# Kernel optimization log

Measured on AMD Instinct MI355X. Metric: run time of the kernel, lower is better.

The kernel has to match this reference:

```python
import jax, jax.numpy as jnp
import numpy as np
from jax import lax

N_CLUSTERS = 512
B = 128


def _extract_windows(sym, k, s):
    # sym: (B, H, W, C) int symbols -> (B, oh, ow, k*k*C); window layout (ki, kj, c)
    Bb, H, W, C = sym.shape
    oh = (H - k) // s + 1
    ow = (W - k) // s + 1
    parts = [sym[:, i:i + s * oh:s, j:j + s * ow:s, :] for i in range(k) for j in range(k)]
    w = jnp.stack(parts, axis=3)  # (B, oh, ow, k*k, C)
    return w.reshape(Bb, oh, ow, k * k * C)


def _conv_reduce(arr, add_lut):
    # Faithful SymConv2D inner reduction: sort window symbols, then sequentially
    # fold through add_lut with the conditional swap-and-resort of the original.
    n = arr.shape[1]
    arr = jnp.sort(arr, axis=1)
    tmp = arr[:, 0]

    def step(carry, j):
        a, t = carry
        t2 = add_lut[a[:, j], t]
        jc = jnp.minimum(j + 1, n - 1)
        nxt = a[:, jc]
        cond = (j < n - 2) & (t2 > nxt)
        a_sw = a.at[:, jc].set(jnp.where(cond, t2, nxt))
        a_new = jnp.where(cond[:, None], jnp.sort(a_sw, axis=1), a)
        t_new = jnp.where(cond, nxt, t2)
        return (a_new, t_new), None

    (_, tmp), _ = lax.scan(step, (arr, tmp), jnp.arange(1, n))
    return tmp


def _fc_reduce(arr, add_lut):
    # SymFC inner reduction: sort once, then plain sequential add_lut fold.
    arr = jnp.sort(arr, axis=1)
    cols = jnp.moveaxis(arr[:, 1:], 1, 0)  # (n-1, R)

    def step(t, col):
        return add_lut[col, t], None

    tmp, _ = lax.scan(step, arr[:, 0], cols)
    return tmp


def _sym_conv(sym, w_sym, conv_lut, add_lut, bias_lut, k=5, s=2):
    # sym: (B, H, W, C) int symbols; w_sym: (k*k*C, Co) kernel symbols
    win = _extract_windows(sym, k, s)  # (B, oh, ow, n)
    Bb, oh, ow, n = win.shape
    Co = w_sym.shape[1]
    # conv_lut gather: pair each window symbol with each output channel's kernel symbol
    g = conv_lut[win[:, :, :, None, :], w_sym.T[None, None, None, :, :]]  # (B, oh, ow, Co, n)
    syms = _conv_reduce(g.reshape(-1, n), add_lut).reshape(Bb, oh, ow, Co)
    return bias_lut[syms, jnp.arange(Co)]


def _sym_fc(x, w_sym, fc_lut, add_lut, bias_lut):
    # x: (B, n) symbols; w_sym: (m, n)
    g = fc_lut[x[:, None, :], w_sym[None, :, :]]  # (B, m, n)
    Bb, m, n = g.shape
    syms = _fc_reduce(g.reshape(-1, n), add_lut).reshape(Bb, m)
    return bias_lut[syms, jnp.arange(m)]


def _discretize(x, centroid_lut):
    # 1x1 patches: nearest-centroid quantization of each pixel
    px = x[:, 0]  # (B, 32, 32)
    d = jnp.abs(px[..., None] - centroid_lut[None, None, None, :, 0])
    return lax.stop_gradient(jnp.argmin(d, axis=-1).astype(jnp.int32))


def setup_inputs() -> dict:
    key = jax.random.key(0)
    ks = jax.random.split(key, 16)
    ri = lambda k, shape: jax.random.randint(k, shape, 0, N_CLUSTERS, dtype=jnp.int32)
    return {
        'x_bat': jax.random.normal(ks[0], (B, 1, 32, 32), jnp.float32),
        'centroid_lut': jax.random.normal(ks[1], (N_CLUSTERS, 1), jnp.float32),
        'conv_lut': ri(ks[2], (N_CLUSTERS, N_CLUSTERS)),
        'fc_lut': ri(ks[3], (N_CLUSTERS, N_CLUSTERS)),
        'add_lut': ri(ks[4], (N_CLUSTERS, N_CLUSTERS)),
        'relu_lut': ri(ks[5], (N_CLUSTERS,)),
        'c1_bias_lut': ri(ks[6], (N_CLUSTERS, 6)),
        'c2_bias_lut': ri(ks[7], (N_CLUSTERS, 16)),
        'f1_bias_lut': ri(ks[8], (N_CLUSTERS, 120)),
        'f2_bias_lut': ri(ks[9], (N_CLUSTERS, 84)),
        'c1f': ri(ks[10], (25, 6)),
        'c2f': ri(ks[11], (150, 16)),
        'f1f': ri(ks[12], (120, 400)),
        'f2f': ri(ks[13], (84, 120)),
        'fc3_w': jax.random.normal(ks[14], (10, 84), jnp.float32) * 0.1,
        'fc3_b': jax.random.normal(ks[15], (10,), jnp.float32) * 0.1,
    }


def reference(x_bat, centroid_lut, conv_lut, fc_lut, add_lut, relu_lut,
              c1_bias_lut, c2_bias_lut, f1_bias_lut, f2_bias_lut,
              c1f, c2f, f1f, f2f, fc3_w, fc3_b):
    x = _discretize(x_bat, centroid_lut)[..., None]              # (B, 32, 32, 1)
    x = _sym_conv(x, c1f, conv_lut, add_lut, c1_bias_lut)        # (B, 14, 14, 6)
    x = relu_lut[x]
    x = _sym_conv(x, c2f, conv_lut, add_lut, c2_bias_lut)        # (B, 5, 5, 16)
    x = relu_lut[x]
    # symbolic_to_symbolic_win with 1x1 patches is identity; channels-first flatten (permute(2,0,1))
    x = jnp.transpose(x, (0, 3, 1, 2)).reshape(x.shape[0], 400)  # (B, 400)
    x = relu_lut[_sym_fc(x, f1f, fc_lut, add_lut, f1_bias_lut)]  # (B, 120)
    x = relu_lut[_sym_fc(x, f2f, fc_lut, add_lut, f2_bias_lut)]  # (B, 84)
    feats = centroid_lut[x, 0]                                   # symbols -> floats, (B, 84)
    logits = feats @ fc3_w.T + fc3_b
    return jax.nn.softmax(logits, axis=1)


if __name__ == '__main__':
    out = reference(**setup_inputs())
    print(out.shape, out.dtype)
```

## Files before the change

### kernel.cpp

```cpp
#include <hip/hip_runtime.h>

#define NC 512

__global__ __launch_bounds__(256) void k_transpose_pack2(
    const int* __restrict__ srcA, unsigned short* __restrict__ dstA,
    const int* __restrict__ srcB, unsigned short* __restrict__ dstB)
{
    __shared__ unsigned short tile[64][65];
    int bid = blockIdx.x & 63;
    const int* src = (blockIdx.x < 64) ? srcA : srcB;
    unsigned short* dst = (blockIdx.x < 64) ? dstA : dstB;
    int tx = bid % 8, ty = bid / 8;
    int lane = threadIdx.x & 63, grp = threadIdx.x >> 6;
    for (int r = grp * 16; r < grp * 16 + 16; ++r)
        tile[r][lane] = (unsigned short)src[(ty * 64 + r) * NC + tx * 64 + lane];
    __syncthreads();
    for (int r = grp * 16; r < grp * 16 + 16; ++r)
        dst[(tx * 64 + r) * NC + ty * 64 + lane] = tile[lane][r];
}

__global__ __launch_bounds__(256) void k_discretize(
    const float* __restrict__ x, const float* __restrict__ cent,
    unsigned short* __restrict__ out)
{
    __shared__ float c[NC];
    int tid = threadIdx.x;
    for (int i = tid; i < NC; i += 256) c[i] = cent[i];
    __syncthreads();
    int id = blockIdx.x * 256 + tid;
    float px = x[id];
    float best = fabsf(px - c[0]);
    int bi = 0;
    for (int k = 1; k < NC; ++k) {
        float d = fabsf(px - c[k]);
        if (d < best) { best = d; bi = k; }
    }
    out[id] = (unsigned short)bi;
}

template<int INST>
struct ScanL {
    uint32_t* col;
    uint64_t w0, w1;
    uint32_t mask;
    int chunk;

    __device__ inline void init(uint32_t* c) { col = c; mask = 0; chunk = -1; }
    __device__ inline void load() {
        uint32_t a0 = col[(chunk * 4 + 0) * INST];
        uint32_t a1 = col[(chunk * 4 + 1) * INST];
        uint32_t a2 = col[(chunk * 4 + 2) * INST];
        uint32_t a3 = col[(chunk * 4 + 3) * INST];
        mask = col[(64 + chunk) * INST];
        w0 = ((uint64_t)a1 << 32) | a0;
        w1 = ((uint64_t)a3 << 32) | a2;
    }
    __device__ inline void ensure() { while (mask == 0) { ++chunk; load(); } }
    __device__ inline int  peek()   { ensure(); return chunk * 32 + (int)__builtin_ctz(mask); }
    __device__ inline void consume_min() {
        int k = (int)__builtin_ctz(mask);
        int sh = (k & 15) << 2;
        bool hi = k >= 16;
        uint64_t cw = hi ? w1 : w0;
        uint32_t cnt = (uint32_t)(cw >> sh) & 0xFu;
        cw -= (1ull << sh);
        if (hi) w1 = cw; else w0 = cw;
        if (cnt == 1) mask &= ~(1u << k);
    }
    __device__ inline int pop() { int v = peek(); consume_min(); return v; }
    __device__ inline void insert(int v) {
        int rel = v - chunk * 32;
        if (rel < 32) {
            int sh = (rel & 15) << 2;
            bool hi = rel >= 16;
            uint64_t cw = hi ? w1 : w0;
            cw += (1ull << sh);
            if (hi) w1 = cw; else w0 = cw;
            mask |= (1u << rel);
        } else {
            col[(v >> 3) * INST] += (1u << ((v & 7) << 2));
            col[(64 + (v >> 5)) * INST] |= (1u << (v & 31));
        }
    }
};

template<typename IT, typename OT, bool KMAJOR, int INST,
         int CIN, int CO, int IH, int IW, int OH, int OW>
__device__ __forceinline__ void conv_body(
    const IT* __restrict__ in_sym,
    const int* __restrict__ wsym,
    const unsigned short* __restrict__ convT,
    const int* __restrict__ add_lut,
    const int* __restrict__ bias_lut,
    const int* __restrict__ relu_lut,
    OT* __restrict__ out)
{
    constexpr int N    = 25 * CIN;
    constexpr int SUB  = 64 / INST;
    constexpr int PPI  = OH * OW;
    constexpr int BPC  = (128 * PPI) / INST;
    __shared__ uint32_t bins[80 * INST];
    int tid = threadIdx.x;
    int il  = tid % INST;
    int sub = tid / INST;

    for (int i = tid; i < 80 * INST; i += 64) bins[i] = 0u;

    int posg = blockIdx.x % BPC;
    int co   = blockIdx.x / BPC;
    int pos  = posg * INST + il;
    int b  = pos / PPI;
    int yx = pos % PPI;
    int oy = yx / OW, ox = yx % OW;
    __syncthreads();

#pragma unroll 4
    for (int n = sub; n < N; n += SUB) {
        int i   = n / (5 * CIN);
        int rem = n % (5 * CIN);
        int j   = rem / CIN;
        int c   = rem % CIN;
        int s = (int)in_sym[((b * IH + (oy * 2 + i)) * IW + (ox * 2 + j)) * CIN + c];
        int w = wsym[n * CO + co];
        int g = convT[w * NC + s];
        atomicAdd(&bins[(g >> 3) * INST + il], 1u << ((g & 7) << 2));
        atomicOr (&bins[(64 + (g >> 5)) * INST + il], 1u << (g & 31));
    }
    __syncthreads();

    ScanL<INST> sc; sc.init(bins + il);
    int t = sc.pop();
    int u = sc.pop();
    int v = sc.pop();
    int t2 = add_lut[u * NC + t];
#pragma unroll 1
    for (int j = 1; j <= N - 3; ++j) {
        int bb = sc.pop();
        bool cA = (t2 <= v);
        bool cC = (t2 > bb);
        t = cA ? t2 : v;
        u = cA ? v : (cC ? bb : t2);
        int t2n = add_lut[u * NC + t];
        __builtin_amdgcn_sched_barrier(0);
        if (cC) { sc.insert(t2); v = sc.pop(); }
        else    v = bb;
        t2 = t2n;
    }
    t = t2;
    t = add_lut[v * NC + t];
    if (sub == 0) {
        int r = relu_lut[bias_lut[t * CO + co]];
        if (KMAJOR) out[(co * PPI + yx) * 128 + b] = (OT)r;
        else        out[pos * CO + co] = (OT)r;
    }
}

__global__ __launch_bounds__(64) void k_conv1(
    const unsigned short* in, const int* wsym, const unsigned short* convT,
    const int* add_lut, const int* bias, const int* relu, unsigned short* out)
{
    conv_body<unsigned short, unsigned short, false, 64, 1, 6, 32, 32, 14, 14>(
        in, wsym, convT, add_lut, bias, relu, out);
}

__global__ __launch_bounds__(64) void k_conv2(
    const unsigned short* in, const int* wsym, const unsigned short* convT,
    const int* add_lut, const int* bias, const int* relu, int* out)
{
    conv_body<unsigned short, int, true, 16, 6, 16, 14, 14, 5, 5>(
        in, wsym, convT, add_lut, bias, relu, out);
}

template<int M, int K>
__device__ __forceinline__ void fc_body(
    const int* __restrict__ in_sym,
    const int* __restrict__ wsym,
    const unsigned short* __restrict__ fcT,
    const int* __restrict__ add_lut,
    const int* __restrict__ bias_lut,
    const int* __restrict__ relu_lut,
    int* __restrict__ out)
{
    constexpr int INST = 8;
    constexpr int SUB  = 8;
    __shared__ uint32_t bins[80 * INST];
    int tid = threadIdx.x;
    int il  = tid % INST;
    int sub = tid / INST;

    for (int i = tid; i < 80 * INST; i += 64) bins[i] = 0u;

    int m  = blockIdx.x / 16;
    int bg = blockIdx.x % 16;
    int b  = bg * INST + il;
    __syncthreads();

#pragma unroll 4
    for (int k = sub; k < K; k += SUB) {
        int x = in_sym[k * 128 + b];
        int w = wsym[m * K + k];
        int g = fcT[w * NC + x];
        atomicAdd(&bins[(g >> 3) * INST + il], 1u << ((g & 7) << 2));
        atomicOr (&bins[(64 + (g >> 5)) * INST + il], 1u << (g & 31));
    }
    __syncthreads();

    ScanL<INST> sc; sc.init(bins + il);
    int t = sc.pop();
    int x = sc.pop();
    int t2 = add_lut[x * NC + t];
#pragma unroll 1
    for (int s = 1; s < K - 1; ++s) {
        int xn = sc.pop();
        t = t2;
        t2 = add_lut[xn * NC + t];
        __builtin_amdgcn_sched_barrier(0);
    }
    t = t2;
    if (sub == 0)
        out[m * 128 + b] = relu_lut[bias_lut[t * M + m]];
}

__global__ __launch_bounds__(64) void k_fc1(
    const int* in, const int* wsym, const unsigned short* fcT,
    const int* add_lut, const int* bias, const int* relu, int* out)
{
    fc_body<120, 400>(in, wsym, fcT, add_lut, bias, relu, out);
}

__global__ __launch_bounds__(64) void k_fc2(
    const int* in, const int* wsym, const unsigned short* fcT,
    const int* add_lut, const int* bias, const int* relu, int* out)
{
    fc_body<84, 120>(in, wsym, fcT, add_lut, bias, relu, out);
}

__global__ __launch_bounds__(64) void k_head(
    const int* __restrict__ f2m,
    const float* __restrict__ cent,
    const float* __restrict__ w,
    const float* __restrict__ bias,
    float* __restrict__ out)
{
    int b = blockIdx.x * 64 + threadIdx.x;
    float acc[10];
#pragma unroll
    for (int o = 0; o < 10; ++o) acc[o] = bias[o];
    for (int k = 0; k < 84; ++k) {
        float f = cent[f2m[k * 128 + b]];
#pragma unroll
        for (int o = 0; o < 10; ++o) acc[o] += f * w[o * 84 + k];
    }
    float mx = acc[0];
#pragma unroll
    for (int o = 1; o < 10; ++o) mx = fmaxf(mx, acc[o]);
    float s = 0.f;
#pragma unroll
    for (int o = 0; o < 10; ++o) { acc[o] = expf(acc[o] - mx); s += acc[o]; }
    float inv = 1.f / s;
#pragma unroll
    for (int o = 0; o < 10; ++o) out[b * 10 + o] = acc[o] * inv;
}

extern "C" void kernel_launch(void* const* d_in, const int* in_sizes, int n_in,
                              void* d_out, int out_size, void* d_ws, size_t ws_size,
                              hipStream_t stream)
{
    const float* x_bat  = (const float*)d_in[0];
    const float* cent   = (const float*)d_in[1];
    const int* conv_lut = (const int*)d_in[2];
    const int* fc_lut   = (const int*)d_in[3];
    const int* add_lut  = (const int*)d_in[4];
    const int* relu_lut = (const int*)d_in[5];
    const int* c1_bias  = (const int*)d_in[6];
    const int* c2_bias  = (const int*)d_in[7];
    const int* f1_bias  = (const int*)d_in[8];
    const int* f2_bias  = (const int*)d_in[9];
    const int* c1f      = (const int*)d_in[10];
    const int* c2f      = (const int*)d_in[11];
    const int* f1f      = (const int*)d_in[12];
    const int* f2f      = (const int*)d_in[13];
    const float* fc3_w  = (const float*)d_in[14];
    const float* fc3_b  = (const float*)d_in[15];
    float* out = (float*)d_out;

    char* ws = (char*)d_ws;
    unsigned short* convT = (unsigned short*)(ws);
    unsigned short* fcT   = (unsigned short*)(ws + 524288);
    unsigned short* sym0  = (unsigned short*)(ws + 1048576);
    unsigned short* c1o   = (unsigned short*)(ws + 1310720);
    int* c2o = (int*)(ws + 1611776);
    int* f1o = (int*)(ws + 1816576);
    int* f2o = (int*)(ws + 1878016);

    k_transpose_pack2<<<128, 256, 0, stream>>>(conv_lut, convT, fc_lut, fcT);
    k_discretize<<<512, 256, 0, stream>>>(x_bat, cent, sym0);
    k_conv1<<<2352, 64, 0, stream>>>(sym0, c1f, convT, add_lut, c1_bias, relu_lut, c1o);
    k_conv2<<<3200, 64, 0, stream>>>(c1o, c2f, convT, add_lut, c2_bias, relu_lut, c2o);
    k_fc1<<<1920, 64, 0, stream>>>(c2o, f1f, fcT, add_lut, f1_bias, relu_lut, f1o);
    k_fc2<<<1344, 64, 0, stream>>>(f1o, f2f, fcT, add_lut, f2_bias, relu_lut, f2o);
    k_head<<<2, 64, 0, stream>>>(f2o, cent, fc3_w, fc3_b, out);
}
```

Baseline: 381.0 us.

## Interleave two independent reduction chains per thread in conv2 and FC kernels

Each thread in conv2, fc1 and fc2 now handles two output instances (A and B) and interleaves their sequential add_lut fold chains. The aim is to hide the latency of the dependent global LUT loads by giving each wavefront two independent chains, while halving the grid sizes. In exchange, each block uses twice the shared memory, registers rise, and there are half as many blocks, which could lower occupancy or leave the GPU underfilled.

```diff
diff --git a/kernel.cpp b/kernel.cpp
--- a/kernel.cpp
+++ b/kernel.cpp
@@ -38,7 +38,7 @@
     out[id] = (unsigned short)bi;
 }
 
-template<int INST>
+template<int STRIDE>
 struct ScanL {
     uint32_t* col;
     uint64_t w0, w1;
@@ -47,11 +47,11 @@
 
     __device__ inline void init(uint32_t* c) { col = c; mask = 0; chunk = -1; }
     __device__ inline void load() {
-        uint32_t a0 = col[(chunk * 4 + 0) * INST];
-        uint32_t a1 = col[(chunk * 4 + 1) * INST];
-        uint32_t a2 = col[(chunk * 4 + 2) * INST];
-        uint32_t a3 = col[(chunk * 4 + 3) * INST];
-        mask = col[(64 + chunk) * INST];
+        uint32_t a0 = col[(chunk * 4 + 0) * STRIDE];
+        uint32_t a1 = col[(chunk * 4 + 1) * STRIDE];
+        uint32_t a2 = col[(chunk * 4 + 2) * STRIDE];
+        uint32_t a3 = col[(chunk * 4 + 3) * STRIDE];
+        mask = col[(64 + chunk) * STRIDE];
         w0 = ((uint64_t)a1 << 32) | a0;
         w1 = ((uint64_t)a3 << 32) | a2;
     }
@@ -78,21 +78,18 @@
             if (hi) w1 = cw; else w0 = cw;
             mask |= (1u << rel);
         } else {
-            col[(v >> 3) * INST] += (1u << ((v & 7) << 2));
-            col[(64 + (v >> 5)) * INST] |= (1u << (v & 31));
+            col[(v >> 3) * STRIDE] += (1u << ((v & 7) << 2));
+            col[(64 + (v >> 5)) * STRIDE] |= (1u << (v & 31));
         }
     }
 };
 
 template<typename IT, typename OT, bool KMAJOR, int INST,
          int CIN, int CO, int IH, int IW, int OH, int OW>
-__device__ __forceinline__ void conv_body(
-    const IT* __restrict__ in_sym,
-    const int* __restrict__ wsym,
-    const unsigned short* __restrict__ convT,
-    const int* __restrict__ add_lut,
-    const int* __restrict__ bias_lut,
-    const int* __restrict__ relu_lut,
+__device__ __forceinline__ void conv_body1(
+    const IT* __restrict__ in_sym, const int* __restrict__ wsym,
+    const unsigned short* __restrict__ convT, const int* __restrict__ add_lut,
+    const int* __restrict__ bias_lut, const int* __restrict__ relu_lut,
     OT* __restrict__ out)
 {
     constexpr int N    = 25 * CIN;
@@ -155,11 +152,99 @@
     }
 }
 
+template<typename IT, typename OT, bool KMAJOR, int INST,
+         int CIN, int CO, int IH, int IW, int OH, int OW>
+__device__ __forceinline__ void conv_body2(
+    const IT* __restrict__ in_sym, const int* __restrict__ wsym,
+    const unsigned short* __restrict__ convT, const int* __restrict__ add_lut,
+    const int* __restrict__ bias_lut, const int* __restrict__ relu_lut,
+    OT* __restrict__ out)
+{
+    constexpr int N    = 25 * CIN;
+    constexpr int SUB  = 64 / INST;
+    constexpr int PPI  = OH * OW;
+    constexpr int CH   = 2 * INST;
+    constexpr int BPC  = (128 * PPI) / CH;
+    __shared__ uint32_t bins[80 * CH];
+    int tid = threadIdx.x;
+    int il  = tid % INST;
+    int sub = tid / INST;
+
+    for (int i = tid; i < 80 * CH; i += 64) bins[i] = 0u;
+
+    int posg = blockIdx.x % BPC;
+    int co   = blockIdx.x / BPC;
+    int posA = posg * CH + il;
+    int posB = posg * CH + INST + il;
+    int bA = posA / PPI, yxA = posA % PPI, oyA = yxA / OW, oxA = yxA % OW;
+    int bB = posB / PPI, yxB = posB % PPI, oyB = yxB / OW, oxB = yxB % OW;
+    __syncthreads();
+
+#pragma unroll 2
+    for (int n = sub; n < N; n += SUB) {
+        int i   = n / (5 * CIN);
+        int rem = n % (5 * CIN);
+        int j   = rem / CIN;
+        int c   = rem % CIN;
+        int w = wsym[n * CO + co];
+        int sA = (int)in_sym[((bA * IH + (oyA * 2 + i)) * IW + (oxA * 2 + j)) * CIN + c];
+        int gA = convT[w * NC + sA];
+        atomicAdd(&bins[(gA >> 3) * CH + il], 1u << ((gA & 7) << 2));
+        atomicOr (&bins[(64 + (gA >> 5)) * CH + il], 1u << (gA & 31));
+        int sB = (int)in_sym[((bB * IH + (oyB * 2 + i)) * IW + (oxB * 2 + j)) * CIN + c];
+        int gB = convT[w * NC + sB];
+        atomicAdd(&bins[(gB >> 3) * CH + INST + il], 1u << ((gB & 7) << 2));
+        atomicOr (&bins[(64 + (gB >> 5)) * CH + INST + il], 1u << (gB & 31));
+    }
+    __syncthreads();
+
+    ScanL<CH> scA; scA.init(bins + il);
+    ScanL<CH> scB; scB.init(bins + INST + il);
+    int tA = scA.pop(), uA = scA.pop(), vA = scA.pop();
+    int t2A = add_lut[uA * NC + tA];
+    int tB = scB.pop(), uB = scB.pop(), vB = scB.pop();
+    int t2B = add_lut[uB * NC + tB];
+#pragma unroll 1
+    for (int j = 1; j <= N - 3; ++j) {
+        int bbA = scA.pop();
+        bool cAA = (t2A <= vA), cCA = (t2A > bbA);
+        tA = cAA ? t2A : vA;
+        uA = cAA ? vA : (cCA ? bbA : t2A);
+        int t2nA = add_lut[uA * NC + tA];
+        __builtin_amdgcn_sched_barrier(0);
+        if (cCA) { scA.insert(t2A); vA = scA.pop(); }
+        else     vA = bbA;
+        t2A = t2nA;
+        int bbB = scB.pop();
+        bool cAB = (t2B <= vB), cCB = (t2B > bbB);
+        tB = cAB ? t2B : vB;
+        uB = cAB ? vB : (cCB ? bbB : t2B);
+        int t2nB = add_lut[uB * NC + tB];
+        __builtin_amdgcn_sched_barrier(0);
+        if (cCB) { scB.insert(t2B); vB = scB.pop(); }
+        else     vB = bbB;
+        t2B = t2nB;
+    }
+    tA = t2A; tA = add_lut[vA * NC + tA];
+    tB = t2B; tB = add_lut[vB * NC + tB];
+    if (sub == 0) {
+        int rA = relu_lut[bias_lut[tA * CO + co]];
+        int rB = relu_lut[bias_lut[tB * CO + co]];
+        if (KMAJOR) {
+            out[(co * PPI + yxA) * 128 + bA] = (OT)rA;
+            out[(co * PPI + yxB) * 128 + bB] = (OT)rB;
+        } else {
+            out[posA * CO + co] = (OT)rA;
+            out[posB * CO + co] = (OT)rB;
+        }
+    }
+}
+
 __global__ __launch_bounds__(64) void k_conv1(
     const unsigned short* in, const int* wsym, const unsigned short* convT,
     const int* add_lut, const int* bias, const int* relu, unsigned short* out)
 {
-    conv_body<unsigned short, unsigned short, false, 64, 1, 6, 32, 32, 14, 14>(
+    conv_body1<unsigned short, unsigned short, false, 64, 1, 6, 32, 32, 14, 14>(
         in, wsym, convT, add_lut, bias, relu, out);
 }
 
@@ -167,7 +252,7 @@
     const unsigned short* in, const int* wsym, const unsigned short* convT,
     const int* add_lut, const int* bias, const int* relu, int* out)
 {
-    conv_body<unsigned short, int, true, 16, 6, 16, 14, 14, 5, 5>(
+    conv_body2<unsigned short, int, true, 16, 6, 16, 14, 14, 5, 5>(
         in, wsym, convT, add_lut, bias, relu, out);
 }
 
@@ -182,43 +267,59 @@
     int* __restrict__ out)
 {
     constexpr int INST = 8;
+    constexpr int CH   = 16;
     constexpr int SUB  = 8;
-    __shared__ uint32_t bins[80 * INST];
+    __shared__ uint32_t bins[80 * CH];
     int tid = threadIdx.x;
     int il  = tid % INST;
     int sub = tid / INST;
 
-    for (int i = tid; i < 80 * INST; i += 64) bins[i] = 0u;
-
-    int m  = blockIdx.x / 16;
-    int bg = blockIdx.x % 16;
-    int b  = bg * INST + il;
-    __syncthreads();
-
-#pragma unroll 4
+    for (int i = tid; i < 80 * CH; i += 64) bins[i] = 0u;
+
+    int m  = blockIdx.x / 8;
+    int bg = blockIdx.x % 8;
+    int bA = bg * CH + il;
+    int bB = bg * CH + INST + il;
+    __syncthreads();
+
+#pragma unroll 2
     for (int k = sub; k < K; k += SUB) {
-        int x = in_sym[k * 128 + b];
         int w = wsym[m * K + k];
-        int g = fcT[w * NC + x];
-        atomicAdd(&bins[(g >> 3) * INST + il], 1u << ((g & 7) << 2));
-        atomicOr (&bins[(64 + (g >> 5)) * INST + il], 1u << (g & 31));
-    }
-    __syncthreads();
-
-    ScanL<INST> sc; sc.init(bins + il);
-    int t = sc.pop();
-    int x = sc.pop();
-    int t2 = add_lut[x * NC + t];
+        int xA = in_sym[k * 128 + bA];
+        int gA = fcT[w * NC + xA];
+        atomicAdd(&bins[(gA >> 3) * CH + il], 1u << ((gA & 7) << 2));
+        atomicOr (&bins[(64 + (gA >> 5)) * CH + il], 1u << (gA & 31));
+        int xB = in_sym[k * 128 + bB];
+        int gB = fcT[w * NC + xB];
+        atomicAdd(&bins[(gB >> 3) * CH + INST + il], 1u << ((gB & 7) << 2));
+        atomicOr (&bins[(64 + (gB >> 5)) * CH + INST + il], 1u << (gB & 31));
+    }
+    __syncthreads();
+
+    ScanL<CH> scA; scA.init(bins + il);
+    ScanL<CH> scB; scB.init(bins + INST + il);
+    int tA = scA.pop();
+    int xA = scA.pop();
+    int t2A = add_lut[xA * NC + tA];
+    int tB = scB.pop();
+    int xB = scB.pop();
+    int t2B = add_lut[xB * NC + tB];
 #pragma unroll 1
     for (int s = 1; s < K - 1; ++s) {
-        int xn = sc.pop();
-        t = t2;
-        t2 = add_lut[xn * NC + t];
+        int xnA = scA.pop();
+        tA = t2A;
+        t2A = add_lut[xnA * NC + tA];
         __builtin_amdgcn_sched_barrier(0);
-    }
-    t = t2;
-    if (sub == 0)
-        out[m * 128 + b] = relu_lut[bias_lut[t * M + m]];
+        int xnB = scB.pop();
+        tB = t2B;
+        t2B = add_lut[xnB * NC + tB];
+        __builtin_amdgcn_sched_barrier(0);
+    }
+    tA = t2A; tB = t2B;
+    if (sub == 0) {
+        out[m * 128 + bA] = relu_lut[bias_lut[tA * M + m]];
+        out[m * 128 + bB] = relu_lut[bias_lut[tB * M + m]];
+    }
 }
 
 __global__ __launch_bounds__(64) void k_fc1(
@@ -296,8 +397,8 @@
     k_transpose_pack2<<<128, 256, 0, stream>>>(conv_lut, convT, fc_lut, fcT);
     k_discretize<<<512, 256, 0, stream>>>(x_bat, cent, sym0);
     k_conv1<<<2352, 64, 0, stream>>>(sym0, c1f, convT, add_lut, c1_bias, relu_lut, c1o);
-    k_conv2<<<3200, 64, 0, stream>>>(c1o, c2f, convT, add_lut, c2_bias, relu_lut, c2o);
-    k_fc1<<<1920, 64, 0, stream>>>(c2o, f1f, fcT, add_lut, f1_bias, relu_lut, f1o);
-    k_fc2<<<1344, 64, 0, stream>>>(f1o, f2f, fcT, add_lut, f2_bias, relu_lut, f2o);
+    k_conv2<<<1600, 64, 0, stream>>>(c1o, c2f, convT, add_lut, c2_bias, relu_lut, c2o);
+    k_fc1<<<960, 64, 0, stream>>>(c2o, f1f, fcT, add_lut, f1_bias, relu_lut, f1o);
+    k_fc2<<<672, 64, 0, stream>>>(f1o, f2f, fcT, add_lut, f2_bias, relu_lut, f2o);
     k_head<<<2, 64, 0, stream>>>(f2o, cent, fc3_w, fc3_b, out);
 }
```

Result: slower. 479.4 us (+25.8%).

## Merge preprocessing kernels and prefetch next histogram chunk in conv scan

Applied to the files above, without the earlier changes.

Fuses the LUT transpose and discretize kernels into one launch split by block index, saving one launch. In the conv reduction, a new scanner prefetches the next 32-symbol chunk of the LDS histogram into registers so the chunk advance does not wait on a fresh LDS read. Out-of-chunk inserts now go through atomics issued only by the leader lane, and the prefetch is refreshed when the insert lands in the next chunk. This adds register pressure and subtle correctness coupling between the lanes that share a histogram column.

```diff
diff --git a/kernel.cpp b/kernel.cpp
--- a/kernel.cpp
+++ b/kernel.cpp
@@ -2,44 +2,44 @@
 
 #define NC 512
 
-__global__ __launch_bounds__(256) void k_transpose_pack2(
+__global__ __launch_bounds__(256) void k_pre(
     const int* __restrict__ srcA, unsigned short* __restrict__ dstA,
-    const int* __restrict__ srcB, unsigned short* __restrict__ dstB)
-{
-    __shared__ unsigned short tile[64][65];
-    int bid = blockIdx.x & 63;
-    const int* src = (blockIdx.x < 64) ? srcA : srcB;
-    unsigned short* dst = (blockIdx.x < 64) ? dstA : dstB;
-    int tx = bid % 8, ty = bid / 8;
-    int lane = threadIdx.x & 63, grp = threadIdx.x >> 6;
-    for (int r = grp * 16; r < grp * 16 + 16; ++r)
-        tile[r][lane] = (unsigned short)src[(ty * 64 + r) * NC + tx * 64 + lane];
-    __syncthreads();
-    for (int r = grp * 16; r < grp * 16 + 16; ++r)
-        dst[(tx * 64 + r) * NC + ty * 64 + lane] = tile[lane][r];
-}
-
-__global__ __launch_bounds__(256) void k_discretize(
+    const int* __restrict__ srcB, unsigned short* __restrict__ dstB,
     const float* __restrict__ x, const float* __restrict__ cent,
-    unsigned short* __restrict__ out)
-{
-    __shared__ float c[NC];
+    unsigned short* __restrict__ outsym)
+{
+    __shared__ __align__(16) char smem[64 * 65 * 2];
     int tid = threadIdx.x;
-    for (int i = tid; i < NC; i += 256) c[i] = cent[i];
-    __syncthreads();
-    int id = blockIdx.x * 256 + tid;
-    float px = x[id];
-    float best = fabsf(px - c[0]);
-    int bi = 0;
-    for (int k = 1; k < NC; ++k) {
-        float d = fabsf(px - c[k]);
-        if (d < best) { best = d; bi = k; }
-    }
-    out[id] = (unsigned short)bi;
-}
-
-template<int INST>
-struct ScanL {
+    if (blockIdx.x < 128) {
+        unsigned short (*tile)[65] = (unsigned short(*)[65])smem;
+        int bid = blockIdx.x & 63;
+        const int* src = (blockIdx.x < 64) ? srcA : srcB;
+        unsigned short* dst = (blockIdx.x < 64) ? dstA : dstB;
+        int tx = bid % 8, ty = bid / 8;
+        int lane = tid & 63, grp = tid >> 6;
+        for (int r = grp * 16; r < grp * 16 + 16; ++r)
+            tile[r][lane] = (unsigned short)src[(ty * 64 + r) * NC + tx * 64 + lane];
+        __syncthreads();
+        for (int r = grp * 16; r < grp * 16 + 16; ++r)
+            dst[(tx * 64 + r) * NC + ty * 64 + lane] = tile[lane][r];
+    } else {
+        float* c = (float*)smem;
+        for (int i = tid; i < NC; i += 256) c[i] = cent[i];
+        __syncthreads();
+        int id = (blockIdx.x - 128) * 256 + tid;
+        float px = x[id];
+        float best = fabsf(px - c[0]);
+        int bi = 0;
+        for (int k = 1; k < NC; ++k) {
+            float d = fabsf(px - c[k]);
+            if (d < best) { best = d; bi = k; }
+        }
+        outsym[id] = (unsigned short)bi;
+    }
+}
+
+template<int STRIDE>
+struct ScanL32 {
     uint32_t* col;
     uint64_t w0, w1;
     uint32_t mask;
@@ -47,11 +47,11 @@
 
     __device__ inline void init(uint32_t* c) { col = c; mask = 0; chunk = -1; }
     __device__ inline void load() {
-        uint32_t a0 = col[(chunk * 4 + 0) * INST];
-        uint32_t a1 = col[(chunk * 4 + 1) * INST];
-        uint32_t a2 = col[(chunk * 4 + 2) * INST];
-        uint32_t a3 = col[(chunk * 4 + 3) * INST];
-        mask = col[(64 + chunk) * INST];
+        uint32_t a0 = col[(chunk * 4 + 0) * STRIDE];
+        uint32_t a1 = col[(chunk * 4 + 1) * STRIDE];
+        uint32_t a2 = col[(chunk * 4 + 2) * STRIDE];
+        uint32_t a3 = col[(chunk * 4 + 3) * STRIDE];
+        mask = col[(64 + chunk) * STRIDE];
         w0 = ((uint64_t)a1 << 32) | a0;
         w1 = ((uint64_t)a3 << 32) | a2;
     }
@@ -68,6 +68,49 @@
         if (cnt == 1) mask &= ~(1u << k);
     }
     __device__ inline int pop() { int v = peek(); consume_min(); return v; }
+};
+
+template<int STRIDE>
+struct ScanP {
+    uint32_t* col;
+    uint64_t w0, w1;
+    uint32_t mask;
+    uint32_t p0, p1, p2, p3, pm;
+    int chunk;
+    bool leader;
+
+    __device__ inline void pf(int nc) {
+        p0 = col[(nc * 4 + 0) * STRIDE];
+        p1 = col[(nc * 4 + 1) * STRIDE];
+        p2 = col[(nc * 4 + 2) * STRIDE];
+        p3 = col[(nc * 4 + 3) * STRIDE];
+        pm = col[(64 + nc) * STRIDE];
+    }
+    __device__ inline void init(uint32_t* c, bool lead) {
+        col = c; leader = lead; mask = 0; chunk = -1;
+        pf(0);
+    }
+    __device__ inline void advance() {
+        ++chunk;
+        w0 = ((uint64_t)p1 << 32) | p0;
+        w1 = ((uint64_t)p3 << 32) | p2;
+        mask = pm;
+        int nc = chunk + 1;
+        if (nc < 16) pf(nc);
+    }
+    __device__ inline void ensure() { while (mask == 0) advance(); }
+    __device__ inline int  peek()   { ensure(); return chunk * 32 + (int)__builtin_ctz(mask); }
+    __device__ inline void consume_min() {
+        int k = (int)__builtin_ctz(mask);
+        int sh = (k & 15) << 2;
+        bool hi = k >= 16;
+        uint64_t cw = hi ? w1 : w0;
+        uint32_t cnt = (uint32_t)(cw >> sh) & 0xFu;
+        cw -= (1ull << sh);
+        if (hi) w1 = cw; else w0 = cw;
+        if (cnt == 1) mask &= ~(1u << k);
+    }
+    __device__ inline int pop() { int v = peek(); consume_min(); return v; }
     __device__ inline void insert(int v) {
         int rel = v - chunk * 32;
         if (rel < 32) {
@@ -78,8 +121,11 @@
             if (hi) w1 = cw; else w0 = cw;
             mask |= (1u << rel);
         } else {
-            col[(v >> 3) * INST] += (1u << ((v & 7) << 2));
-            col[(64 + (v >> 5)) * INST] |= (1u << (v & 31));
+            if (leader) {
+                atomicAdd(&col[(v >> 3) * STRIDE], 1u << ((v & 7) << 2));
+                atomicOr (&col[(64 + (v >> 5)) * STRIDE], 1u << (v & 31));
+            }
+            if (rel < 64) pf(chunk + 1);
         }
     }
 };
@@ -128,7 +174,7 @@
     }
     __syncthreads();
 
-    ScanL<INST> sc; sc.init(bins + il);
+    ScanP<INST> sc; sc.init(bins + il, sub == 0);
     int t = sc.pop();
     int u = sc.pop();
     int v = sc.pop();
@@ -205,7 +251,7 @@
     }
     __syncthreads();
 
-    ScanL<INST> sc; sc.init(bins + il);
+    ScanL32<INST> sc; sc.init(bins + il);
     int t = sc.pop();
     int x = sc.pop();
     int t2 = add_lut[x * NC + t];
@@ -293,8 +339,7 @@
     int* f1o = (int*)(ws + 1816576);
     int* f2o = (int*)(ws + 1878016);
 
-    k_transpose_pack2<<<128, 256, 0, stream>>>(conv_lut, convT, fc_lut, fcT);
-    k_discretize<<<512, 256, 0, stream>>>(x_bat, cent, sym0);
+    k_pre<<<640, 256, 0, stream>>>(conv_lut, convT, fc_lut, fcT, x_bat, cent, sym0);
     k_conv1<<<2352, 64, 0, stream>>>(sym0, c1f, convT, add_lut, c1_bias, relu_lut, c1o);
     k_conv2<<<3200, 64, 0, stream>>>(c1o, c2f, convT, add_lut, c2_bias, relu_lut, c2o);
     k_fc1<<<1920, 64, 0, stream>>>(c2o, f1f, fcT, add_lut, f1_bias, relu_lut, f1o);
```

Measured after the change: 392.1 us. 1.03x slower.

## Merge preprocessing kernels and speculate add_lut lookup in conv reduction loop

Applied to the files above, without the earlier changes.

Combines the LUT transpose and discretize kernels into one launch with shared-memory aliasing, removing one kernel launch. In the conv reduction loop, the add_lut lookup for the swap case (bb, v) is issued before the branch condition is known, and the non-swap lookup is moved into the else branch. This shortens the dependent-latency chain when the swap path is taken, at the cost of an extra load per iteration and divergent lookups between lanes. The ScanL template parameter is renamed from INST to STRIDE.

```diff
diff --git a/kernel.cpp b/kernel.cpp
--- a/kernel.cpp
+++ b/kernel.cpp
@@ -2,43 +2,43 @@
 
 #define NC 512
 
-__global__ __launch_bounds__(256) void k_transpose_pack2(
+__global__ __launch_bounds__(256) void k_pre(
     const int* __restrict__ srcA, unsigned short* __restrict__ dstA,
-    const int* __restrict__ srcB, unsigned short* __restrict__ dstB)
-{
-    __shared__ unsigned short tile[64][65];
-    int bid = blockIdx.x & 63;
-    const int* src = (blockIdx.x < 64) ? srcA : srcB;
-    unsigned short* dst = (blockIdx.x < 64) ? dstA : dstB;
-    int tx = bid % 8, ty = bid / 8;
-    int lane = threadIdx.x & 63, grp = threadIdx.x >> 6;
-    for (int r = grp * 16; r < grp * 16 + 16; ++r)
-        tile[r][lane] = (unsigned short)src[(ty * 64 + r) * NC + tx * 64 + lane];
-    __syncthreads();
-    for (int r = grp * 16; r < grp * 16 + 16; ++r)
-        dst[(tx * 64 + r) * NC + ty * 64 + lane] = tile[lane][r];
-}
-
-__global__ __launch_bounds__(256) void k_discretize(
+    const int* __restrict__ srcB, unsigned short* __restrict__ dstB,
     const float* __restrict__ x, const float* __restrict__ cent,
-    unsigned short* __restrict__ out)
-{
-    __shared__ float c[NC];
+    unsigned short* __restrict__ outsym)
+{
+    __shared__ __align__(16) char smem[64 * 65 * 2];
     int tid = threadIdx.x;
-    for (int i = tid; i < NC; i += 256) c[i] = cent[i];
-    __syncthreads();
-    int id = blockIdx.x * 256 + tid;
-    float px = x[id];
-    float best = fabsf(px - c[0]);
-    int bi = 0;
-    for (int k = 1; k < NC; ++k) {
-        float d = fabsf(px - c[k]);
-        if (d < best) { best = d; bi = k; }
-    }
-    out[id] = (unsigned short)bi;
-}
-
-template<int INST>
+    if (blockIdx.x < 128) {
+        unsigned short (*tile)[65] = (unsigned short(*)[65])smem;
+        int bid = blockIdx.x & 63;
+        const int* src = (blockIdx.x < 64) ? srcA : srcB;
+        unsigned short* dst = (blockIdx.x < 64) ? dstA : dstB;
+        int tx = bid % 8, ty = bid / 8;
+        int lane = tid & 63, grp = tid >> 6;
+        for (int r = grp * 16; r < grp * 16 + 16; ++r)
+            tile[r][lane] = (unsigned short)src[(ty * 64 + r) * NC + tx * 64 + lane];
+        __syncthreads();
+        for (int r = grp * 16; r < grp * 16 + 16; ++r)
+            dst[(tx * 64 + r) * NC + ty * 64 + lane] = tile[lane][r];
+    } else {
+        float* c = (float*)smem;
+        for (int i = tid; i < NC; i += 256) c[i] = cent[i];
+        __syncthreads();
+        int id = (blockIdx.x - 128) * 256 + tid;
+        float px = x[id];
+        float best = fabsf(px - c[0]);
+        int bi = 0;
+        for (int k = 1; k < NC; ++k) {
+            float d = fabsf(px - c[k]);
+            if (d < best) { best = d; bi = k; }
+        }
+        outsym[id] = (unsigned short)bi;
+    }
+}
+
+template<int STRIDE>
 struct ScanL {
     uint32_t* col;
     uint64_t w0, w1;
@@ -47,11 +47,11 @@
 
     __device__ inline void init(uint32_t* c) { col = c; mask = 0; chunk = -1; }
     __device__ inline void load() {
-        uint32_t a0 = col[(chunk * 4 + 0) * INST];
-        uint32_t a1 = col[(chunk * 4 + 1) * INST];
-        uint32_t a2 = col[(chunk * 4 + 2) * INST];
-        uint32_t a3 = col[(chunk * 4 + 3) * INST];
-        mask = col[(64 + chunk) * INST];
+        uint32_t a0 = col[(chunk * 4 + 0) * STRIDE];
+        uint32_t a1 = col[(chunk * 4 + 1) * STRIDE];
+        uint32_t a2 = col[(chunk * 4 + 2) * STRIDE];
+        uint32_t a3 = col[(chunk * 4 + 3) * STRIDE];
+        mask = col[(64 + chunk) * STRIDE];
         w0 = ((uint64_t)a1 << 32) | a0;
         w1 = ((uint64_t)a3 << 32) | a2;
     }
@@ -78,8 +78,8 @@
             if (hi) w1 = cw; else w0 = cw;
             mask |= (1u << rel);
         } else {
-            col[(v >> 3) * INST] += (1u << ((v & 7) << 2));
-            col[(64 + (v >> 5)) * INST] |= (1u << (v & 31));
+            col[(v >> 3) * STRIDE] += (1u << ((v & 7) << 2));
+            col[(64 + (v >> 5)) * STRIDE] |= (1u << (v & 31));
         }
     }
 };
@@ -136,15 +136,19 @@
 #pragma unroll 1
     for (int j = 1; j <= N - 3; ++j) {
         int bb = sc.pop();
+        int spec = add_lut[bb * NC + v];
+        __builtin_amdgcn_sched_barrier(0);
         bool cA = (t2 <= v);
         bool cC = (t2 > bb);
         t = cA ? t2 : v;
         u = cA ? v : (cC ? bb : t2);
-        int t2n = add_lut[u * NC + t];
-        __builtin_amdgcn_sched_barrier(0);
-        if (cC) { sc.insert(t2); v = sc.pop(); }
-        else    v = bb;
-        t2 = t2n;
+        if (cC) {
+            sc.insert(t2); v = sc.pop();
+            t2 = spec;
+        } else {
+            t2 = add_lut[u * NC + t];
+            v = bb;
+        }
     }
     t = t2;
     t = add_lut[v * NC + t];
@@ -293,8 +297,7 @@
     int* f1o = (int*)(ws + 1816576);
     int* f2o = (int*)(ws + 1878016);
 
-    k_transpose_pack2<<<128, 256, 0, stream>>>(conv_lut, convT, fc_lut, fcT);
-    k_discretize<<<512, 256, 0, stream>>>(x_bat, cent, sym0);
+    k_pre<<<640, 256, 0, stream>>>(conv_lut, convT, fc_lut, fcT, x_bat, cent, sym0);
     k_conv1<<<2352, 64, 0, stream>>>(sym0, c1f, convT, add_lut, c1_bias, relu_lut, c1o);
     k_conv2<<<3200, 64, 0, stream>>>(c1o, c2f, convT, add_lut, c2_bias, relu_lut, c2o);
     k_fc1<<<1920, 64, 0, stream>>>(c2o, f1f, fcT, add_lut, f1_bias, relu_lut, f1o);
```

After: 380.4 us. Within noise of the previous version (-0.1%).
